# Kernel tuning notes

Measured on AMD Instinct MI355X. Metric: run time of the kernel, lower is better.

The kernel has to match this reference:

```python
import jax, jax.numpy as jnp
import numpy as np

N = 50000      # nodes
E = 800000     # edges (avg degree 16)
D = 64         # hidden_dim = heads * per-head channels
H = 4          # heads
C = D // H     # per-head channels
EDIM = 16      # edge feature dim
L = 3          # num_layers
NEG_SLOPE = 0.2


def setup_inputs() -> dict:
    key = jax.random.key(0)
    ks = jax.random.split(key, 11)
    s = 0.1
    return {
        "x": jax.random.normal(ks[0], (N, D), dtype=jnp.float32),
        "edge_index": jax.random.randint(ks[1], (2, E), 0, N, dtype=jnp.int32),
        "edge_attr": jax.random.normal(ks[2], (E, EDIM), dtype=jnp.float32),
        # stacked per-layer GATv2 parameters (all layers have in=out=D)
        "Wl": jax.random.normal(ks[3], (L, D, D), dtype=jnp.float32) * s,
        "bl": jnp.zeros((L, D), dtype=jnp.float32),
        "Wr": jax.random.normal(ks[4], (L, D, D), dtype=jnp.float32) * s,
        "br": jnp.zeros((L, D), dtype=jnp.float32),
        "We": jax.random.normal(ks[5], (L, EDIM, D), dtype=jnp.float32) * s,
        "att": jax.random.normal(ks[6], (L, H, C), dtype=jnp.float32) * s,
        "bias": jnp.zeros((L, D), dtype=jnp.float32),
    }


def _gatv2_layer(x, src, dst, edge_attr, Wl, bl, Wr, br, We, att, bias):
    # x: [N, D] -> out: [N, D] (concat of H heads of C channels)
    xl = (x @ Wl + bl).reshape(N, H, C)          # source transform (message value)
    xr = (x @ Wr + br).reshape(N, H, C)          # target transform
    ef = (edge_attr @ We).reshape(E, H, C)       # edge feature transform
    m = jax.nn.leaky_relu(xl[src] + xr[dst] + ef, NEG_SLOPE)  # [E, H, C]
    score = jnp.einsum('ehc,hc->eh', m, att)     # [E, H]
    # segment softmax over incoming edges of each target node
    smax = jax.ops.segment_max(score, dst, num_segments=N)   # [N, H]
    ex = jnp.exp(score - smax[dst])                          # [E, H]
    denom = jax.ops.segment_sum(ex, dst, num_segments=N)     # [N, H]
    alpha = ex / denom[dst]                                  # [E, H]
    out = jax.ops.segment_sum(alpha[:, :, None] * xl[src], dst, num_segments=N)
    return out.reshape(N, D) + bias


def reference(x, edge_index, edge_attr, Wl, bl, Wr, br, We, att, bias):
    src, dst = edge_index[0], edge_index[1]
    h = x
    for l in range(L):
        h = _gatv2_layer(h, src, dst, edge_attr,
                         Wl[l], bl[l], Wr[l], br[l], We[l], att[l], bias[l])
        h = jax.nn.relu(h)
    return h
```

## Files before the change

kernel.cpp:

```cpp
#include <hip/hip_runtime.h>
#include <cfloat>

#define NEG_SLOPE 0.2f

__global__ __launch_bounds__(256) void zero_kernel(int* __restrict__ counts,
                                                   int* __restrict__ cursor, int n) {
    int gid = blockIdx.x * 256 + threadIdx.x;
    if (gid < n) { counts[gid] = 0; cursor[gid] = 0; }
}

__global__ __launch_bounds__(256) void count_kernel(const int* __restrict__ dst,
                                                    int* __restrict__ counts, int E) {
    int e = blockIdx.x * 256 + threadIdx.x;
    if (e < E) atomicAdd(&counts[dst[e]], 1);
}

__global__ __launch_bounds__(256) void scan_bsums_kernel(const int* __restrict__ counts,
                                                         int* __restrict__ bsums, int N) {
    int t = threadIdx.x;
    int base = blockIdx.x * 1024 + t * 4;
    int s = 0;
    #pragma unroll
    for (int i = 0; i < 4; ++i) { int idx = base + i; if (idx < N) s += counts[idx]; }
    #pragma unroll
    for (int d = 1; d < 64; d <<= 1) s += __shfl_xor(s, d);
    __shared__ int ws[4];
    if ((t & 63) == 0) ws[t >> 6] = s;
    __syncthreads();
    if (t == 0) bsums[blockIdx.x] = ws[0] + ws[1] + ws[2] + ws[3];
}

__global__ __launch_bounds__(64) void scan_bscan_kernel(int* __restrict__ bsums, int NB) {
    int t = threadIdx.x;
    int v = (t < NB) ? bsums[t] : 0;
    int x = v;
    #pragma unroll
    for (int d = 1; d < 64; d <<= 1) {
        int y = __shfl_up(x, d);
        if (t >= d) x += y;
    }
    if (t < NB) bsums[t] = x - v;
}

__global__ __launch_bounds__(256) void scan_final_kernel(const int* __restrict__ counts,
                                                         const int* __restrict__ bsums,
                                                         int* __restrict__ offs, int N) {
    int t = threadIdx.x, lane = t & 63, w = t >> 6;
    int base = blockIdx.x * 1024 + t * 4;
    int v[4]; int s = 0;
    #pragma unroll
    for (int i = 0; i < 4; ++i) { int idx = base + i; v[i] = (idx < N) ? counts[idx] : 0; s += v[i]; }
    int x = s;
    #pragma unroll
    for (int d = 1; d < 64; d <<= 1) {
        int y = __shfl_up(x, d);
        if (lane >= d) x += y;
    }
    __shared__ int wtot[4];
    if (lane == 63) wtot[w] = x;
    __syncthreads();
    int wexc = 0;
    for (int i = 0; i < w; ++i) wexc += wtot[i];
    int run = (x - s) + wexc + bsums[blockIdx.x];
    #pragma unroll
    for (int i = 0; i < 4; ++i) {
        int idx = base + i;
        run += v[i];
        if (idx < N) offs[idx + 1] = run;
    }
    if (blockIdx.x == 0 && t == 0) offs[0] = 0;
}

__global__ __launch_bounds__(256) void scatter_kernel(
    const int* __restrict__ src, const int* __restrict__ dst,
    const int* __restrict__ offs, int* __restrict__ cursor,
    int4* __restrict__ csr, int E) {
    int base = (blockIdx.x * 256 + threadIdx.x) * 8;
    if (base >= E) return;
    int n = E - base; if (n > 8) n = 8;
    int s0[8], d0[8], p0[8];
    #pragma unroll
    for (int i = 0; i < 8; ++i) {
        if (i < n) { s0[i] = src[base + i]; d0[i] = dst[base + i]; }
    }
    #pragma unroll
    for (int i = 0; i < 8; ++i) {
        if (i < n) p0[i] = offs[d0[i]] + atomicAdd(&cursor[d0[i]], 1);
    }
    #pragma unroll
    for (int i = 0; i < 8; ++i) {
        if (i < n) csr[p0[i]] = make_int4(s0[i], d0[i], base + i, 0);
    }
}

__global__ __launch_bounds__(256) void sort_segments_kernel(
    int4* __restrict__ csr, const int* __restrict__ offs, int N)
{
    int t = threadIdx.x;
    int lane = t & 63;
    int node = blockIdx.x * 4 + (t >> 6);
    if (node >= N) return;
    int off = offs[node];
    int deg = offs[node + 1] - off;
    if (deg <= 1) return;
    if (deg <= 64) {
        int key = 0x7FFFFFFF; int4 kv = make_int4(0, 0, 0, 0);
        if (lane < deg) { kv = csr[off + lane]; key = kv.z; }
        int rank = 0;
        #pragma unroll
        for (int i = 0; i < 64; ++i) {
            int ki = __shfl(key, i);
            if (ki < key) rank++;
        }
        if (lane < deg) csr[off + rank] = kv;
    } else if (lane == 0) {
        for (int a = 1; a < deg; ++a) {
            int4 kv = csr[off + a];
            int b = a - 1;
            while (b >= 0 && csr[off + b].z > kv.z) {
                csr[off + b + 1] = csr[off + b];
                b--;
            }
            csr[off + b + 1] = kv;
        }
    }
}

#define XSTRIDE 68
__global__ __launch_bounds__(256) void node_gemm_kernel(
    const float* __restrict__ hin,
    const float* __restrict__ Wl, const float* __restrict__ bl,
    const float* __restrict__ Wr, const float* __restrict__ br,
    float* __restrict__ xl, float* __restrict__ xr, int nrows)
{
    __shared__ float sWl[4096];
    __shared__ float sWr[4096];
    __shared__ float sX[64 * XSTRIDE];
    int t = threadIdx.x;
    {
        float4* dl = (float4*)sWl; const float4* sl = (const float4*)Wl;
        float4* dr = (float4*)sWr; const float4* sr = (const float4*)Wr;
        for (int i = t; i < 1024; i += 256) { dl[i] = sl[i]; dr[i] = sr[i]; }
    }
    int row0 = blockIdx.x * 64;
    for (int i = t; i < 1024; i += 256) {
        int rr = i >> 4;
        int cc = (i & 15) << 2;
        int row = row0 + rr;
        float4 v = make_float4(0.f, 0.f, 0.f, 0.f);
        if (row < nrows) v = *(const float4*)(hin + (size_t)row * 64 + cc);
        *(float4*)(&sX[rr * XSTRIDE + cc]) = v;
    }
    __syncthreads();

    int lane = t & 63;
    int w = t >> 6;
    int rs = lane >> 4;
    int c4 = lane & 15;
    int rbase = w * 16 + rs * 4;

    float4 al0 = {0,0,0,0}, al1 = {0,0,0,0}, al2 = {0,0,0,0}, al3 = {0,0,0,0};
    float4 ar0 = {0,0,0,0}, ar1 = {0,0,0,0}, ar2 = {0,0,0,0}, ar3 = {0,0,0,0};
    const float* x0p = &sX[(rbase + 0) * XSTRIDE];
    const float* x1p = &sX[(rbase + 1) * XSTRIDE];
    const float* x2p = &sX[(rbase + 2) * XSTRIDE];
    const float* x3p = &sX[(rbase + 3) * XSTRIDE];

    #pragma unroll 4
    for (int k = 0; k < 64; ++k) {
        float4 wl4 = *(const float4*)(&sWl[k * 64 + c4 * 4]);
        float4 wr4 = *(const float4*)(&sWr[k * 64 + c4 * 4]);
        float xk0 = x0p[k], xk1 = x1p[k], xk2 = x2p[k], xk3 = x3p[k];
        al0.x += xk0 * wl4.x; al0.y += xk0 * wl4.y; al0.z += xk0 * wl4.z; al0.w += xk0 * wl4.w;
        al1.x += xk1 * wl4.x; al1.y += xk1 * wl4.y; al1.z += xk1 * wl4.z; al1.w += xk1 * wl4.w;
        al2.x += xk2 * wl4.x; al2.y += xk2 * wl4.y; al2.z += xk2 * wl4.z; al2.w += xk2 * wl4.w;
        al3.x += xk3 * wl4.x; al3.y += xk3 * wl4.y; al3.z += xk3 * wl4.z; al3.w += xk3 * wl4.w;
        ar0.x += xk0 * wr4.x; ar0.y += xk0 * wr4.y; ar0.z += xk0 * wr4.z; ar0.w += xk0 * wr4.w;
        ar1.x += xk1 * wr4.x; ar1.y += xk1 * wr4.y; ar1.z += xk1 * wr4.z; ar1.w += xk1 * wr4.w;
        ar2.x += xk2 * wr4.x; ar2.y += xk2 * wr4.y; ar2.z += xk2 * wr4.z; ar2.w += xk2 * wr4.w;
        ar3.x += xk3 * wr4.x; ar3.y += xk3 * wr4.y; ar3.z += xk3 * wr4.z; ar3.w += xk3 * wr4.w;
    }

    float4 bl4 = *(const float4*)(bl + c4 * 4);
    float4 br4 = *(const float4*)(br + c4 * 4);
    #pragma unroll
    for (int r = 0; r < 4; ++r) {
        int row = row0 + rbase + r;
        if (row >= nrows) break;
        float4 av = (r == 0) ? al0 : (r == 1) ? al1 : (r == 2) ? al2 : al3;
        float4 bv = (r == 0) ? ar0 : (r == 1) ? ar1 : (r == 2) ? ar2 : ar3;
        float4 ol, orr;
        ol.x = av.x + bl4.x; ol.y = av.y + bl4.y; ol.z = av.z + bl4.z; ol.w = av.w + bl4.w;
        orr.x = bv.x + br4.x; orr.y = bv.y + br4.y; orr.z = bv.z + br4.z; orr.w = bv.w + br4.w;
        *(float4*)(xl + (size_t)row * 64 + c4 * 4) = ol;
        *(float4*)(xr + (size_t)row * 64 + c4 * 4) = orr;
    }
}

__global__ __launch_bounds__(256) void edge_score_kernel(
    const float* __restrict__ xl, const float* __restrict__ xr,
    const float* __restrict__ ea,
    const int4* __restrict__ csr,
    const float* __restrict__ We, const float* __restrict__ att,
    float* __restrict__ score_csr, int E)
{
    __shared__ float sWe[1024];
    __shared__ float sAtt[64];
    int t = threadIdx.x;
    for (int i = t; i < 1024; i += 256) sWe[i] = We[i];
    if (t < 64) sAtt[t] = att[t];
    __syncthreads();
    int gid = blockIdx.x * 256 + t;
    int pos = gid >> 2, h = gid & 3;
    if (pos >= E) return;
    int4 se = csr[pos];
    int s = se.x, d = se.y;
    const float4* eap = (const float4*)(ea + (size_t)se.z * 16);
    float4 a0 = eap[0], a1 = eap[1], a2 = eap[2], a3 = eap[3];
    float av[16] = {a0.x, a0.y, a0.z, a0.w, a1.x, a1.y, a1.z, a1.w,
                    a2.x, a2.y, a2.z, a2.w, a3.x, a3.y, a3.z, a3.w};
    const float4* xls = (const float4*)(xl + (size_t)s * 64 + h * 16);
    const float4* xrd = (const float4*)(xr + (size_t)d * 64 + h * 16);
    float4 vl0 = xls[0], vl1 = xls[1], vl2 = xls[2], vl3 = xls[3];
    float4 vr0 = xrd[0], vr1 = xrd[1], vr2 = xrd[2], vr3 = xrd[3];

    float4 ef0 = {0.f,0.f,0.f,0.f}, ef1 = {0.f,0.f,0.f,0.f};
    float4 ef2 = {0.f,0.f,0.f,0.f}, ef3 = {0.f,0.f,0.f,0.f};
    #pragma unroll
    for (int k = 0; k < 16; ++k) {
        float a = av[k];
        const float4* w4 = (const float4*)(&sWe[k * 64 + h * 16]);
        float4 w0 = w4[0], w1 = w4[1], w2 = w4[2], w3 = w4[3];
        ef0.x += a * w0.x; ef0.y += a * w0.y; ef0.z += a * w0.z; ef0.w += a * w0.w;
        ef1.x += a * w1.x; ef1.y += a * w1.y; ef1.z += a * w1.z; ef1.w += a * w1.w;
        ef2.x += a * w2.x; ef2.y += a * w2.y; ef2.z += a * w2.z; ef2.w += a * w2.w;
        ef3.x += a * w3.x; ef3.y += a * w3.y; ef3.z += a * w3.z; ef3.w += a * w3.w;
    }

    const float4* at4 = (const float4*)(&sAtt[h * 16]);
    float4 at0 = at4[0], at1 = at4[1], at2 = at4[2], at3 = at4[3];

    float sc0 = 0.f, sc1 = 0.f, sc2 = 0.f, sc3 = 0.f;
    {
        float m0 = vl0.x + vr0.x + ef0.x; m0 = (m0 >= 0.f) ? m0 : NEG_SLOPE * m0;
        float m1 = vl0.y + vr0.y + ef0.y; m1 = (m1 >= 0.f) ? m1 : NEG_SLOPE * m1;
        float m2 = vl0.z + vr0.z + ef0.z; m2 = (m2 >= 0.f) ? m2 : NEG_SLOPE * m2;
        float m3 = vl0.w + vr0.w + ef0.w; m3 = (m3 >= 0.f) ? m3 : NEG_SLOPE * m3;
        sc0 += m0 * at0.x; sc1 += m1 * at0.y; sc2 += m2 * at0.z; sc3 += m3 * at0.w;
    }
    {
        float m0 = vl1.x + vr1.x + ef1.x; m0 = (m0 >= 0.f) ? m0 : NEG_SLOPE * m0;
        float m1 = vl1.y + vr1.y + ef1.y; m1 = (m1 >= 0.f) ? m1 : NEG_SLOPE * m1;
        float m2 = vl1.z + vr1.z + ef1.z; m2 = (m2 >= 0.f) ? m2 : NEG_SLOPE * m2;
        float m3 = vl1.w + vr1.w + ef1.w; m3 = (m3 >= 0.f) ? m3 : NEG_SLOPE * m3;
        sc0 += m0 * at1.x; sc1 += m1 * at1.y; sc2 += m2 * at1.z; sc3 += m3 * at1.w;
    }
    {
        float m0 = vl2.x + vr2.x + ef2.x; m0 = (m0 >= 0.f) ? m0 : NEG_SLOPE * m0;
        float m1 = vl2.y + vr2.y + ef2.y; m1 = (m1 >= 0.f) ? m1 : NEG_SLOPE * m1;
        float m2 = vl2.z + vr2.z + ef2.z; m2 = (m2 >= 0.f) ? m2 : NEG_SLOPE * m2;
        float m3 = vl2.w + vr2.w + ef2.w; m3 = (m3 >= 0.f) ? m3 : NEG_SLOPE * m3;
        sc0 += m0 * at2.x; sc1 += m1 * at2.y; sc2 += m2 * at2.z; sc3 += m3 * at2.w;
    }
    {
        float m0 = vl3.x + vr3.x + ef3.x; m0 = (m0 >= 0.f) ? m0 : NEG_SLOPE * m0;
        float m1 = vl3.y + vr3.y + ef3.y; m1 = (m1 >= 0.f) ? m1 : NEG_SLOPE * m1;
        float m2 = vl3.z + vr3.z + ef3.z; m2 = (m2 >= 0.f) ? m2 : NEG_SLOPE * m2;
        float m3 = vl3.w + vr3.w + ef3.w; m3 = (m3 >= 0.f) ? m3 : NEG_SLOPE * m3;
        sc0 += m0 * at3.x; sc1 += m1 * at3.y; sc2 += m2 * at3.z; sc3 += m3 * at3.w;
    }
    score_csr[gid] = (sc0 + sc1) + (sc2 + sc3);
}

__global__ __launch_bounds__(256) void node_pass_kernel(
    const float* __restrict__ score_csr, const float* __restrict__ xl,
    const int4* __restrict__ csr,
    const int* __restrict__ offs, const float* __restrict__ bias,
    float* __restrict__ hout, int N)
{
    int t = threadIdx.x;
    int lane = t & 63;
    int node = blockIdx.x * 4 + (t >> 6);
    if (node >= N) return;
    int eg = lane >> 4;
    int k  = lane & 15;
    int h  = k >> 2;
    int off = offs[node];
    int deg = offs[node + 1] - off;

    if (deg == 0) {
        if (eg == 0) {
            float4 b = *(const float4*)(bias + k * 4);
            float4 o;
            o.x = fmaxf(b.x, 0.f); o.y = fmaxf(b.y, 0.f);
            o.z = fmaxf(b.z, 0.f); o.w = fmaxf(b.w, 0.f);
            *(float4*)(hout + (size_t)node * 64 + k * 4) = o;
        }
        return;
    }

    float mx = -FLT_MAX;
    for (int j0 = 0; j0 < deg; j0 += 4) {
        int j = j0 + eg;
        if (j < deg) {
            float sc = score_csr[(size_t)(off + j) * 4 + h];
            mx = fmaxf(mx, sc);
        }
    }
    mx = fmaxf(mx, __shfl_xor(mx, 16));
    mx = fmaxf(mx, __shfl_xor(mx, 32));

    float4 acc = {0.f, 0.f, 0.f, 0.f};
    float sSum = 0.f;
    for (int j0 = 0; j0 < deg; j0 += 4) {
        int j = j0 + eg;
        int jj = (j < deg) ? j : deg - 1;
        int pos = off + jj;
        int s = csr[pos].x;
        float sc = score_csr[(size_t)pos * 4 + h];
        float ex = (j < deg) ? __expf(sc - mx) : 0.f;
        float4 v = *(const float4*)(xl + (size_t)s * 64 + k * 4);
        acc.x += ex * v.x; acc.y += ex * v.y;
        acc.z += ex * v.z; acc.w += ex * v.w;
        sSum += ex;
    }

    acc.x += __shfl_xor(acc.x, 16); acc.y += __shfl_xor(acc.y, 16);
    acc.z += __shfl_xor(acc.z, 16); acc.w += __shfl_xor(acc.w, 16);
    sSum  += __shfl_xor(sSum, 16);
    acc.x += __shfl_xor(acc.x, 32); acc.y += __shfl_xor(acc.y, 32);
    acc.z += __shfl_xor(acc.z, 32); acc.w += __shfl_xor(acc.w, 32);
    sSum  += __shfl_xor(sSum, 32);

    if (eg == 0) {
        float inv = 1.f / sSum;
        float4 b = *(const float4*)(bias + k * 4);
        float4 o;
        o.x = fmaxf(acc.x * inv + b.x, 0.f);
        o.y = fmaxf(acc.y * inv + b.y, 0.f);
        o.z = fmaxf(acc.z * inv + b.z, 0.f);
        o.w = fmaxf(acc.w * inv + b.w, 0.f);
        *(float4*)(hout + (size_t)node * 64 + k * 4) = o;
    }
}

extern "C" void kernel_launch(void* const* d_in, const int* in_sizes, int n_in,
                              void* d_out, int out_size, void* d_ws, size_t ws_size,
                              hipStream_t stream) {
    const float* x    = (const float*)d_in[0];
    const int*   eidx = (const int*)d_in[1];
    const float* ea   = (const float*)d_in[2];
    const float* Wl   = (const float*)d_in[3];
    const float* bl   = (const float*)d_in[4];
    const float* Wr   = (const float*)d_in[5];
    const float* br   = (const float*)d_in[6];
    const float* We   = (const float*)d_in[7];
    const float* att  = (const float*)d_in[8];
    const float* bias = (const float*)d_in[9];
    float* out = (float*)d_out;

    const int N = in_sizes[0] / 64;
    const int E = in_sizes[1] / 2;
    const int* src = eidx;
    const int* dst = eidx + E;

    float* ws = (float*)d_ws;
    float* xl      = ws;
    float* xr      = xl + (size_t)N * 64;
    float* score   = xr + (size_t)N * 64;
    float* h_tmp   = score + (size_t)E * 4;
    int* counts    = (int*)(h_tmp + (size_t)N * 64);
    int* cursor    = counts + N;
    int* offs      = cursor + N;
    int* bsums     = offs + N + 1;
    uintptr_t p    = (uintptr_t)(bsums + 64);
    p = (p + 15) & ~(uintptr_t)15;
    int4* csr      = (int4*)p;

    dim3 blk(256);
    int g_n    = (N + 255) / 256;
    int g_e    = (E + 255) / 256;
    int g_e8   = (E + 2047) / 2048;
    int g_eh   = (E * 4 + 255) / 256;
    int g_gemm = (N + 63) / 64;
    int g_node = (N + 3) / 4;
    int NB     = (N + 1023) / 1024;

    zero_kernel<<<g_n, blk, 0, stream>>>(counts, cursor, N);
    count_kernel<<<g_e, blk, 0, stream>>>(dst, counts, E);
    scan_bsums_kernel<<<NB, blk, 0, stream>>>(counts, bsums, N);
    scan_bscan_kernel<<<1, 64, 0, stream>>>(bsums, NB);
    scan_final_kernel<<<NB, blk, 0, stream>>>(counts, bsums, offs, N);
    scatter_kernel<<<g_e8, blk, 0, stream>>>(src, dst, offs, cursor, csr, E);
    sort_segments_kernel<<<g_node, blk, 0, stream>>>(csr, offs, N);

    const float* hin = x;
    for (int l = 0; l < 3; ++l) {
        float* hout = (l == 2) ? out : h_tmp;
        node_gemm_kernel<<<g_gemm, blk, 0, stream>>>(hin, Wl + (size_t)l * 4096, bl + l * 64,
                                                     Wr + (size_t)l * 4096, br + l * 64, xl, xr, N);
        edge_score_kernel<<<g_eh, blk, 0, stream>>>(xl, xr, ea, csr,
                                                    We + (size_t)l * 1024, att + l * 64,
                                                    score, E);
        node_pass_kernel<<<g_node, blk, 0, stream>>>(score, xl, csr, offs,
                                                     bias + l * 64, hout, N);
        hin = hout;
    }
}
```

Baseline: 494.6 us.

## Use online softmax in node pass and two edges per thread in scoring

The node aggregation kernel switches from a two-pass segment softmax (max pass, then exp/accumulate pass) to a single-pass online softmax with rescaling, merged across edge groups by shuffle. This removes the second read of the scores and the masked padding work, at the cost of two extra exps per edge. The edge score kernel now launches half as many threads, each computing two edges half the array apart, to amortize the shared-memory weight load and expose more memory-level parallelism. The cost is fewer waves and more registers per thread.

```diff
diff --git a/kernel.cpp b/kernel.cpp
--- a/kernel.cpp
+++ b/kernel.cpp
@@ -197,6 +197,57 @@
     }
 }
 
+__device__ __forceinline__ float edge_score_one(
+    const float* __restrict__ xl, const float* __restrict__ xr,
+    const float* __restrict__ ea, const int4* __restrict__ csr,
+    const float* sWe, const float* sAtt, int pos, int h)
+{
+    int4 se = csr[pos];
+    const float4* eap = (const float4*)(ea + (size_t)se.z * 16);
+    float4 a0 = eap[0], a1 = eap[1], a2 = eap[2], a3 = eap[3];
+    float av[16] = {a0.x, a0.y, a0.z, a0.w, a1.x, a1.y, a1.z, a1.w,
+                    a2.x, a2.y, a2.z, a2.w, a3.x, a3.y, a3.z, a3.w};
+    const float4* xls = (const float4*)(xl + (size_t)se.x * 64 + h * 16);
+    const float4* xrd = (const float4*)(xr + (size_t)se.y * 64 + h * 16);
+    float4 vl0 = xls[0], vl1 = xls[1], vl2 = xls[2], vl3 = xls[3];
+    float4 vr0 = xrd[0], vr1 = xrd[1], vr2 = xrd[2], vr3 = xrd[3];
+
+    float4 ef0 = {0.f,0.f,0.f,0.f}, ef1 = {0.f,0.f,0.f,0.f};
+    float4 ef2 = {0.f,0.f,0.f,0.f}, ef3 = {0.f,0.f,0.f,0.f};
+    #pragma unroll
+    for (int k = 0; k < 16; ++k) {
+        float a = av[k];
+        const float4* w4 = (const float4*)(&sWe[k * 64 + h * 16]);
+        float4 w0 = w4[0], w1 = w4[1], w2 = w4[2], w3 = w4[3];
+        ef0.x += a * w0.x; ef0.y += a * w0.y; ef0.z += a * w0.z; ef0.w += a * w0.w;
+        ef1.x += a * w1.x; ef1.y += a * w1.y; ef1.z += a * w1.z; ef1.w += a * w1.w;
+        ef2.x += a * w2.x; ef2.y += a * w2.y; ef2.z += a * w2.z; ef2.w += a * w2.w;
+        ef3.x += a * w3.x; ef3.y += a * w3.y; ef3.z += a * w3.z; ef3.w += a * w3.w;
+    }
+
+    const float4* at4 = (const float4*)(&sAtt[h * 16]);
+    float4 at0 = at4[0], at1 = at4[1], at2 = at4[2], at3 = at4[3];
+    float sc0 = 0.f, sc1 = 0.f, sc2 = 0.f, sc3 = 0.f;
+    float q;
+    q = vl0.x + vr0.x + ef0.x; q = (q >= 0.f) ? q : NEG_SLOPE * q; sc0 += q * at0.x;
+    q = vl0.y + vr0.y + ef0.y; q = (q >= 0.f) ? q : NEG_SLOPE * q; sc1 += q * at0.y;
+    q = vl0.z + vr0.z + ef0.z; q = (q >= 0.f) ? q : NEG_SLOPE * q; sc2 += q * at0.z;
+    q = vl0.w + vr0.w + ef0.w; q = (q >= 0.f) ? q : NEG_SLOPE * q; sc3 += q * at0.w;
+    q = vl1.x + vr1.x + ef1.x; q = (q >= 0.f) ? q : NEG_SLOPE * q; sc0 += q * at1.x;
+    q = vl1.y + vr1.y + ef1.y; q = (q >= 0.f) ? q : NEG_SLOPE * q; sc1 += q * at1.y;
+    q = vl1.z + vr1.z + ef1.z; q = (q >= 0.f) ? q : NEG_SLOPE * q; sc2 += q * at1.z;
+    q = vl1.w + vr1.w + ef1.w; q = (q >= 0.f) ? q : NEG_SLOPE * q; sc3 += q * at1.w;
+    q = vl2.x + vr2.x + ef2.x; q = (q >= 0.f) ? q : NEG_SLOPE * q; sc0 += q * at2.x;
+    q = vl2.y + vr2.y + ef2.y; q = (q >= 0.f) ? q : NEG_SLOPE * q; sc1 += q * at2.y;
+    q = vl2.z + vr2.z + ef2.z; q = (q >= 0.f) ? q : NEG_SLOPE * q; sc2 += q * at2.z;
+    q = vl2.w + vr2.w + ef2.w; q = (q >= 0.f) ? q : NEG_SLOPE * q; sc3 += q * at2.w;
+    q = vl3.x + vr3.x + ef3.x; q = (q >= 0.f) ? q : NEG_SLOPE * q; sc0 += q * at3.x;
+    q = vl3.y + vr3.y + ef3.y; q = (q >= 0.f) ? q : NEG_SLOPE * q; sc1 += q * at3.y;
+    q = vl3.z + vr3.z + ef3.z; q = (q >= 0.f) ? q : NEG_SLOPE * q; sc2 += q * at3.z;
+    q = vl3.w + vr3.w + ef3.w; q = (q >= 0.f) ? q : NEG_SLOPE * q; sc3 += q * at3.w;
+    return (sc0 + sc1) + (sc2 + sc3);
+}
+
 __global__ __launch_bounds__(256) void edge_score_kernel(
     const float* __restrict__ xl, const float* __restrict__ xr,
     const float* __restrict__ ea,
@@ -210,66 +261,17 @@
     for (int i = t; i < 1024; i += 256) sWe[i] = We[i];
     if (t < 64) sAtt[t] = att[t];
     __syncthreads();
+    int HALF = (E + 1) >> 1;
     int gid = blockIdx.x * 256 + t;
     int pos = gid >> 2, h = gid & 3;
-    if (pos >= E) return;
-    int4 se = csr[pos];
-    int s = se.x, d = se.y;
-    const float4* eap = (const float4*)(ea + (size_t)se.z * 16);
-    float4 a0 = eap[0], a1 = eap[1], a2 = eap[2], a3 = eap[3];
-    float av[16] = {a0.x, a0.y, a0.z, a0.w, a1.x, a1.y, a1.z, a1.w,
-                    a2.x, a2.y, a2.z, a2.w, a3.x, a3.y, a3.z, a3.w};
-    const float4* xls = (const float4*)(xl + (size_t)s * 64 + h * 16);
-    const float4* xrd = (const float4*)(xr + (size_t)d * 64 + h * 16);
-    float4 vl0 = xls[0], vl1 = xls[1], vl2 = xls[2], vl3 = xls[3];
-    float4 vr0 = xrd[0], vr1 = xrd[1], vr2 = xrd[2], vr3 = xrd[3];
-
-    float4 ef0 = {0.f,0.f,0.f,0.f}, ef1 = {0.f,0.f,0.f,0.f};
-    float4 ef2 = {0.f,0.f,0.f,0.f}, ef3 = {0.f,0.f,0.f,0.f};
-    #pragma unroll
-    for (int k = 0; k < 16; ++k) {
-        float a = av[k];
-        const float4* w4 = (const float4*)(&sWe[k * 64 + h * 16]);
-        float4 w0 = w4[0], w1 = w4[1], w2 = w4[2], w3 = w4[3];
-        ef0.x += a * w0.x; ef0.y += a * w0.y; ef0.z += a * w0.z; ef0.w += a * w0.w;
-        ef1.x += a * w1.x; ef1.y += a * w1.y; ef1.z += a * w1.z; ef1.w += a * w1.w;
-        ef2.x += a * w2.x; ef2.y += a * w2.y; ef2.z += a * w2.z; ef2.w += a * w2.w;
-        ef3.x += a * w3.x; ef3.y += a * w3.y; ef3.z += a * w3.z; ef3.w += a * w3.w;
-    }
-
-    const float4* at4 = (const float4*)(&sAtt[h * 16]);
-    float4 at0 = at4[0], at1 = at4[1], at2 = at4[2], at3 = at4[3];
-
-    float sc0 = 0.f, sc1 = 0.f, sc2 = 0.f, sc3 = 0.f;
-    {
-        float m0 = vl0.x + vr0.x + ef0.x; m0 = (m0 >= 0.f) ? m0 : NEG_SLOPE * m0;
-        float m1 = vl0.y + vr0.y + ef0.y; m1 = (m1 >= 0.f) ? m1 : NEG_SLOPE * m1;
-        float m2 = vl0.z + vr0.z + ef0.z; m2 = (m2 >= 0.f) ? m2 : NEG_SLOPE * m2;
-        float m3 = vl0.w + vr0.w + ef0.w; m3 = (m3 >= 0.f) ? m3 : NEG_SLOPE * m3;
-        sc0 += m0 * at0.x; sc1 += m1 * at0.y; sc2 += m2 * at0.z; sc3 += m3 * at0.w;
-    }
-    {
-        float m0 = vl1.x + vr1.x + ef1.x; m0 = (m0 >= 0.f) ? m0 : NEG_SLOPE * m0;
-        float m1 = vl1.y + vr1.y + ef1.y; m1 = (m1 >= 0.f) ? m1 : NEG_SLOPE * m1;
-        float m2 = vl1.z + vr1.z + ef1.z; m2 = (m2 >= 0.f) ? m2 : NEG_SLOPE * m2;
-        float m3 = vl1.w + vr1.w + ef1.w; m3 = (m3 >= 0.f) ? m3 : NEG_SLOPE * m3;
-        sc0 += m0 * at1.x; sc1 += m1 * at1.y; sc2 += m2 * at1.z; sc3 += m3 * at1.w;
-    }
-    {
-        float m0 = vl2.x + vr2.x + ef2.x; m0 = (m0 >= 0.f) ? m0 : NEG_SLOPE * m0;
-        float m1 = vl2.y + vr2.y + ef2.y; m1 = (m1 >= 0.f) ? m1 : NEG_SLOPE * m1;
-        float m2 = vl2.z + vr2.z + ef2.z; m2 = (m2 >= 0.f) ? m2 : NEG_SLOPE * m2;
-        float m3 = vl2.w + vr2.w + ef2.w; m3 = (m3 >= 0.f) ? m3 : NEG_SLOPE * m3;
-        sc0 += m0 * at2.x; sc1 += m1 * at2.y; sc2 += m2 * at2.z; sc3 += m3 * at2.w;
-    }
-    {
-        float m0 = vl3.x + vr3.x + ef3.x; m0 = (m0 >= 0.f) ? m0 : NEG_SLOPE * m0;
-        float m1 = vl3.y + vr3.y + ef3.y; m1 = (m1 >= 0.f) ? m1 : NEG_SLOPE * m1;
-        float m2 = vl3.z + vr3.z + ef3.z; m2 = (m2 >= 0.f) ? m2 : NEG_SLOPE * m2;
-        float m3 = vl3.w + vr3.w + ef3.w; m3 = (m3 >= 0.f) ? m3 : NEG_SLOPE * m3;
-        sc0 += m0 * at3.x; sc1 += m1 * at3.y; sc2 += m2 * at3.z; sc3 += m3 * at3.w;
-    }
-    score_csr[gid] = (sc0 + sc1) + (sc2 + sc3);
+    if (pos >= HALF) return;
+    int pos2 = pos + HALF;
+    float s1 = edge_score_one(xl, xr, ea, csr, sWe, sAtt, pos, h);
+    score_csr[(size_t)pos * 4 + h] = s1;
+    if (pos2 < E) {
+        float s2 = edge_score_one(xl, xr, ea, csr, sWe, sAtt, pos2, h);
+        score_csr[(size_t)pos2 * 4 + h] = s2;
+    }
 }
 
 __global__ __launch_bounds__(256) void node_pass_kernel(
@@ -299,38 +301,40 @@
         return;
     }
 
-    float mx = -FLT_MAX;
+    float m = -FLT_MAX, sSum = 0.f;
+    float4 acc = {0.f, 0.f, 0.f, 0.f};
     for (int j0 = 0; j0 < deg; j0 += 4) {
         int j = j0 + eg;
         if (j < deg) {
-            float sc = score_csr[(size_t)(off + j) * 4 + h];
-            mx = fmaxf(mx, sc);
+            int pos = off + j;
+            int s = csr[pos].x;
+            float sc = score_csr[(size_t)pos * 4 + h];
+            float4 v = *(const float4*)(xl + (size_t)s * 64 + k * 4);
+            float nm = fmaxf(m, sc);
+            float cs = __expf(m - nm);
+            float p  = __expf(sc - nm);
+            sSum = sSum * cs + p;
+            acc.x = acc.x * cs + p * v.x; acc.y = acc.y * cs + p * v.y;
+            acc.z = acc.z * cs + p * v.z; acc.w = acc.w * cs + p * v.w;
+            m = nm;
         }
     }
-    mx = fmaxf(mx, __shfl_xor(mx, 16));
-    mx = fmaxf(mx, __shfl_xor(mx, 32));
-
-    float4 acc = {0.f, 0.f, 0.f, 0.f};
-    float sSum = 0.f;
-    for (int j0 = 0; j0 < deg; j0 += 4) {
-        int j = j0 + eg;
-        int jj = (j < deg) ? j : deg - 1;
-        int pos = off + jj;
-        int s = csr[pos].x;
-        float sc = score_csr[(size_t)pos * 4 + h];
-        float ex = (j < deg) ? __expf(sc - mx) : 0.f;
-        float4 v = *(const float4*)(xl + (size_t)s * 64 + k * 4);
-        acc.x += ex * v.x; acc.y += ex * v.y;
-        acc.z += ex * v.z; acc.w += ex * v.w;
-        sSum += ex;
-    }
-
-    acc.x += __shfl_xor(acc.x, 16); acc.y += __shfl_xor(acc.y, 16);
-    acc.z += __shfl_xor(acc.z, 16); acc.w += __shfl_xor(acc.w, 16);
-    sSum  += __shfl_xor(sSum, 16);
-    acc.x += __shfl_xor(acc.x, 32); acc.y += __shfl_xor(acc.y, 32);
-    acc.z += __shfl_xor(acc.z, 32); acc.w += __shfl_xor(acc.w, 32);
-    sSum  += __shfl_xor(sSum, 32);
+
+    #pragma unroll
+    for (int st = 16; st < 64; st <<= 1) {
+        float mo = __shfl_xor(m, st);
+        float so = __shfl_xor(sSum, st);
+        float4 vo;
+        vo.x = __shfl_xor(acc.x, st); vo.y = __shfl_xor(acc.y, st);
+        vo.z = __shfl_xor(acc.z, st); vo.w = __shfl_xor(acc.w, st);
+        float nm = fmaxf(m, mo);
+        float cs = __expf(m - nm);
+        float co = __expf(mo - nm);
+        sSum = sSum * cs + so * co;
+        acc.x = acc.x * cs + vo.x * co; acc.y = acc.y * cs + vo.y * co;
+        acc.z = acc.z * cs + vo.z * co; acc.w = acc.w * cs + vo.w * co;
+        m = nm;
+    }
 
     if (eg == 0) {
         float inv = 1.f / sSum;
@@ -381,7 +385,8 @@
     int g_n    = (N + 255) / 256;
     int g_e    = (E + 255) / 256;
     int g_e8   = (E + 2047) / 2048;
-    int g_eh   = (E * 4 + 255) / 256;
+    int HALF   = (E + 1) / 2;
+    int g_eh2  = (HALF * 4 + 255) / 256;
     int g_gemm = (N + 63) / 64;
     int g_node = (N + 3) / 4;
     int NB     = (N + 1023) / 1024;
@@ -399,9 +404,9 @@
         float* hout = (l == 2) ? out : h_tmp;
         node_gemm_kernel<<<g_gemm, blk, 0, stream>>>(hin, Wl + (size_t)l * 4096, bl + l * 64,
                                                      Wr + (size_t)l * 4096, br + l * 64, xl, xr, N);
-        edge_score_kernel<<<g_eh, blk, 0, stream>>>(xl, xr, ea, csr,
-                                                    We + (size_t)l * 1024, att + l * 64,
-                                                    score, E);
+        edge_score_kernel<<<g_eh2, blk, 0, stream>>>(xl, xr, ea, csr,
+                                                     We + (size_t)l * 1024, att + l * 64,
+                                                     score, E);
         node_pass_kernel<<<g_node, blk, 0, stream>>>(score, xl, csr, offs,
                                                      bias + l * 64, hout, N);
         hin = hout;
```

Measured after the change: 639.9 us. +29.4%, slower.
